# Optimization experiments

Measured on AMD Instinct MI355X. Metric: run time of the kernel, lower is better.

## Reference

```python
import jax, jax.numpy as jnp
import numpy as np

B, L, N, D, H = 8, 2048, 512, 1024, 16
Hd = D // H
EPS = 1e-5


def layer_norm(x, g, b):
    m = jnp.mean(x, axis=-1, keepdims=True)
    v = jnp.mean(jnp.square(x - m), axis=-1, keepdims=True)
    return (x - m) * jax.lax.rsqrt(v + EPS) * g + b


def setup_inputs() -> dict:
    key = jax.random.key(0)
    ks = jax.random.split(key, 8)
    text = jax.random.normal(ks[0], (B, L, D), dtype=jnp.float32)
    regions = jax.random.normal(ks[1], (B, N, D), dtype=jnp.float32)
    region_mask = jax.random.randint(ks[2], (B, N), 0, 2).astype(bool)
    s = 1.0 / np.sqrt(D)
    Wq = jax.random.normal(ks[3], (D, D), dtype=jnp.float32) * s
    Wk = jax.random.normal(ks[4], (D, D), dtype=jnp.float32) * s
    Wv = jax.random.normal(ks[5], (D, D), dtype=jnp.float32) * s
    Wo = jax.random.normal(ks[6], (D, D), dtype=jnp.float32) * s
    bo = jnp.zeros((D,), dtype=jnp.float32)
    gq = jnp.ones((D,), dtype=jnp.float32)
    bq = jnp.zeros((D,), dtype=jnp.float32)
    gkv = jnp.ones((D,), dtype=jnp.float32)
    bkv = jnp.zeros((D,), dtype=jnp.float32)
    return {"text": text, "regions": regions, "region_mask": region_mask,
            "Wq": Wq, "Wk": Wk, "Wv": Wv, "Wo": Wo, "bo": bo,
            "gq": gq, "bq": bq, "gkv": gkv, "bkv": bkv}


def reference(text, regions, region_mask, Wq, Wk, Wv, Wo, bo, gq, bq, gkv, bkv):
    scale = Hd ** -0.5
    # pre-norm on text (Q) and regions (K only; V uses raw regions, as in source)
    q = layer_norm(text, gq, bq) @ Wq.T            # (B, L, D)
    k = layer_norm(regions, gkv, bkv) @ Wk.T       # (B, N, D)
    v = regions @ Wv.T                              # (B, N, D)
    q = q.reshape(B, L, H, Hd).transpose(0, 2, 1, 3)   # (B, H, L, Hd)
    k = k.reshape(B, N, H, Hd).transpose(0, 2, 1, 3)   # (B, H, N, Hd)
    v = v.reshape(B, N, H, Hd).transpose(0, 2, 1, 3)   # (B, H, N, Hd)
    logits = jnp.einsum('bhld,bhnd->bhln', q, k) * scale
    logits = jnp.where(region_mask[:, None, None, :], logits, -jnp.inf)
    attn = jax.nn.softmax(logits, axis=-1)
    attn = jnp.nan_to_num(attn, nan=0.0)  # all-masked rows -> zeros
    # dropout is identity in eval mode
    out = jnp.einsum('bhln,bhnd->bhld', attn, v)
    out = out.transpose(0, 2, 1, 3).reshape(B, L, D)
    return text + out @ Wo.T + bo
```

## Files before the change

kernel.cpp:

```cpp
#include <hip/hip_runtime.h>

#define SC_L2E 0.180336880111120f

typedef _Float16 half8v __attribute__((ext_vector_type(8)));
typedef _Float16 half4v __attribute__((ext_vector_type(4)));
typedef _Float16 half2v __attribute__((ext_vector_type(2)));
typedef float f32x4 __attribute__((ext_vector_type(4)));
typedef float f32x16 __attribute__((ext_vector_type(16)));

#if __has_builtin(__builtin_amdgcn_exp2f)
#define EXP2(x) __builtin_amdgcn_exp2f(x)
#else
#define EXP2(x) exp2f(x)
#endif

#if __has_builtin(__builtin_amdgcn_cvt_pkrtz)
#define CVTPK(a, b) __builtin_amdgcn_cvt_pkrtz((a), (b))
#else
static __device__ __forceinline__ half2v cvtpk_fb(float a, float b) {
  half2v h; h[0] = (_Float16)a; h[1] = (_Float16)b; return h;
}
#define CVTPK cvtpk_fb
#endif

#define FMAX3(a, b, c) fmaxf(fmaxf((a), (b)), (c))

#define SWZ_OFF(row, lg) ((row) * 32 + ((((lg) ^ (((row) >> 1) & 3))) * 8))

__device__ __forceinline__ void gload_lds16(const void* g, void* l) {
  __builtin_amdgcn_global_load_lds(
      (const __attribute__((address_space(1))) void*)g,
      (__attribute__((address_space(3))) void*)l, 16, 0, 0);
}

__global__ __launch_bounds__(256) void prep_all_kernel(
    const float* __restrict__ W0, const float* __restrict__ W1,
    const float* __restrict__ W2, const float* __restrict__ W3,
    _Float16* __restrict__ Wout, const float* __restrict__ text,
    const float* __restrict__ gq, const float* __restrict__ bq,
    _Float16* __restrict__ Tout, const float* __restrict__ regions,
    const float* __restrict__ gkv, const float* __restrict__ bkv,
    _Float16* __restrict__ Rln, _Float16* __restrict__ Rraw,
    const unsigned char* __restrict__ mask, int* __restrict__ flag) {
  const int blk = blockIdx.x;
  const int t = threadIdx.x;
  if (blk < 2048) {
    const int i = blk * 256 + t;
    const int rgn = i >> 17;
    const float* W = (rgn == 0) ? W0 : (rgn == 1) ? W1 : (rgn == 2) ? W2 : W3;
    const int loc = i & 131071;
    const float4 a  = ((const float4*)W)[loc * 2];
    const float4 b2 = ((const float4*)W)[loc * 2 + 1];
    half8v y;
    y[0] = (_Float16)a.x;  y[1] = (_Float16)a.y;
    y[2] = (_Float16)a.z;  y[3] = (_Float16)a.w;
    y[4] = (_Float16)b2.x; y[5] = (_Float16)b2.y;
    y[6] = (_Float16)b2.z; y[7] = (_Float16)b2.w;
    ((half8v*)Wout)[i] = y;
  } else if (blk < 22528) {
    const bool is_text = blk < 18432;
    const int row = is_text ? (blk - 2048) : (blk - 18432);
    const float* X = is_text ? text : regions;
    const float* ga = is_text ? gq : gkv;
    const float* be = is_text ? bq : bkv;
    const float4 x = ((const float4*)(X + (size_t)row * 1024))[t];
    float s  = x.x + x.y + x.z + x.w;
    float ss = x.x * x.x + x.y * x.y + x.z * x.z + x.w * x.w;
#pragma unroll
    for (int off = 32; off > 0; off >>= 1) {
      s  += __shfl_down(s, off);
      ss += __shfl_down(ss, off);
    }
    __shared__ float red[8];
    __shared__ float smu, srs;
    if ((t & 63) == 0) { red[(t >> 6) * 2] = s; red[(t >> 6) * 2 + 1] = ss; }
    __syncthreads();
    if (t == 0) {
      const float S  = red[0] + red[2] + red[4] + red[6];
      const float SS = red[1] + red[3] + red[5] + red[7];
      const float mm = S * (1.f / 1024.f);
      const float vv = SS * (1.f / 1024.f) - mm * mm;
      smu = mm; srs = rsqrtf(vv + 1e-5f);
    }
    __syncthreads();
    const float mu = smu, rs = srs;
    const float4 g  = ((const float4*)ga)[t];
    const float4 bb = ((const float4*)be)[t];
    half4v y;
    y[0] = (_Float16)((x.x - mu) * rs * g.x + bb.x);
    y[1] = (_Float16)((x.y - mu) * rs * g.y + bb.y);
    y[2] = (_Float16)((x.z - mu) * rs * g.z + bb.z);
    y[3] = (_Float16)((x.w - mu) * rs * g.w + bb.w);
    if (is_text) {
      ((half4v*)(Tout + (size_t)row * 1024))[t] = y;
    } else {
      half4v yr;
      yr[0] = (_Float16)x.x; yr[1] = (_Float16)x.y;
      yr[2] = (_Float16)x.z; yr[3] = (_Float16)x.w;
      ((half4v*)(Rln + (size_t)row * 1024))[t] = y;
      ((half4v*)(Rraw + (size_t)row * 1024))[t] = yr;
    }
  } else {
    __shared__ int sany;
    if (t == 0) sany = 0;
    __syncthreads();
    int any = 0;
    for (int i = t; i < 8 * 512; i += 256)
      if ((i & 3) != 0 && mask[i] != 0) any = 1;
    if (any) sany = 1;
    __syncthreads();
    if (t == 0) *flag = sany;
  }
}

template <int EPI>
__global__ __launch_bounds__(512) void hgemm_big(
    const _Float16* __restrict__ A, const _Float16* __restrict__ W,
    void* __restrict__ Yv, const float* __restrict__ bias,
    const float* __restrict__ resid) {
  __shared__ _Float16 As[32768];
  __shared__ _Float16 Bs[32768];
  const int tid = threadIdx.x;
  const int wg = blockIdx.x;
  const int bm = (wg & 7) * 8 + (wg >> 5);
  const int bn = (wg >> 3) & 3;
  const int wid = tid >> 6, lane = tid & 63;
  const int wr = wid >> 2, wc = wid & 3;
  const int l15 = lane & 15, lg = lane >> 4;

  const int c0 = tid, c1 = tid + 512;
  const int sc0 = ((c0 & 3) ^ ((c0 >> 3) & 3)) * 8;
  const int sc1 = ((c1 & 3) ^ ((c1 >> 3) & 3)) * 8;
  const _Float16* Ag0 = A + (size_t)(bm * 256 + (c0 >> 2)) * 1024 + sc0;
  const _Float16* Ag1 = A + (size_t)(bm * 256 + (c1 >> 2)) * 1024 + sc1;
  const _Float16* Bg0 = W + (size_t)(bn * 256 + (c0 >> 2)) * 1024 + sc0;
  const _Float16* Bg1 = W + (size_t)(bn * 256 + (c1 >> 2)) * 1024 + sc1;
  _Float16* Asl0 = &As[wid * 512];
  _Float16* Asl1 = &As[4096 + wid * 512];
  _Float16* Bsl0 = &Bs[wid * 512];
  _Float16* Bsl1 = &Bs[4096 + wid * 512];

  auto stage = [&](int tk, int bi) {
    const int off = tk * 32;
    gload_lds16(Ag0 + off, Asl0 + bi * 8192);
    gload_lds16(Ag1 + off, Asl1 + bi * 8192);
    gload_lds16(Bg0 + off, Bsl0 + bi * 8192);
    gload_lds16(Bg1 + off, Bsl1 + bi * 8192);
  };

  f32x4 acc[8][4] = {};
  auto compute = [&](int t) {
    const _Float16* Ab = &As[(t & 3) * 8192];
    const _Float16* Bb = &Bs[(t & 3) * 8192];
    half8v a[8], b[4];
#pragma unroll
    for (int m = 0; m < 8; m++) {
      const int row = wr * 128 + m * 16 + l15;
      a[m] = *(const half8v*)&Ab[SWZ_OFF(row, lg)];
    }
#pragma unroll
    for (int n = 0; n < 4; n++) {
      const int row = wc * 64 + n * 16 + l15;
      b[n] = *(const half8v*)&Bb[SWZ_OFF(row, lg)];
    }
    __builtin_amdgcn_s_setprio(1);
#pragma unroll
    for (int m = 0; m < 8; m++)
#pragma unroll
      for (int n = 0; n < 4; n++)
        acc[m][n] = __builtin_amdgcn_mfma_f32_16x16x32_f16(a[m], b[n], acc[m][n], 0, 0, 0);
    __builtin_amdgcn_s_setprio(0);
  };

  stage(0, 0);
  stage(1, 1);
  for (int t = 0; t < 30; ++t) {
    stage(t + 2, (t + 2) & 3);
    asm volatile("s_waitcnt vmcnt(8)" ::: "memory");
    __builtin_amdgcn_sched_barrier(0);
    __builtin_amdgcn_s_barrier();
    compute(t);
  }
  asm volatile("s_waitcnt vmcnt(4)" ::: "memory");
  __builtin_amdgcn_sched_barrier(0);
  __builtin_amdgcn_s_barrier();
  compute(30);
  asm volatile("s_waitcnt vmcnt(0)" ::: "memory");
  __builtin_amdgcn_sched_barrier(0);
  __builtin_amdgcn_s_barrier();
  compute(31);

  if (EPI == 0) {
    _Float16* Y = (_Float16*)Yv;
#pragma unroll
    for (int m = 0; m < 8; m++) {
      const int gr0 = bm * 256 + wr * 128 + m * 16 + lg * 4;
#pragma unroll
      for (int n = 0; n < 4; n++) {
        const int gc = bn * 256 + wc * 64 + n * 16 + l15;
#pragma unroll
        for (int r = 0; r < 4; r++)
          Y[(size_t)(gr0 + r) * 1024 + gc] = (_Float16)(acc[m][n][r] * SC_L2E);
      }
    }
  } else {
    float* Y = (float*)Yv;
#pragma unroll
    for (int m = 0; m < 8; m++) {
      const int gr0 = bm * 256 + wr * 128 + m * 16 + lg * 4;
#pragma unroll
      for (int n = 0; n < 4; n++) {
        const int gc = bn * 256 + wc * 64 + n * 16 + l15;
        const float bv = bias[gc];
#pragma unroll
        for (int r = 0; r < 4; r++)
          Y[(size_t)(gr0 + r) * 1024 + gc] =
              acc[m][n][r] + bv + resid[(size_t)(gr0 + r) * 1024 + gc];
      }
    }
  }
}

__global__ __launch_bounds__(256) void hgemm_kv(
    const _Float16* __restrict__ Aln, const _Float16* __restrict__ Araw,
    const _Float16* __restrict__ Wk, const _Float16* __restrict__ Wv,
    _Float16* __restrict__ Yk, _Float16* __restrict__ YvT) {
  __shared__ _Float16 As[16384];
  __shared__ _Float16 Bs[16384];
  const int z = blockIdx.z;
  const _Float16* A = z ? Araw : Aln;
  const _Float16* W = z ? Wv : Wk;
  const int tid = threadIdx.x;
  const int bm = blockIdx.x, bn = blockIdx.y;
  const int wid = tid >> 6, lane = tid & 63;
  const int wr = wid >> 1, wc = wid & 1;
  const int l15 = lane & 15, lg = lane >> 4;

  const int c0 = tid, c1 = tid + 256;
  const int sc0 = ((c0 & 3) ^ ((c0 >> 3) & 3)) * 8;
  const int sc1 = ((c1 & 3) ^ ((c1 >> 3) & 3)) * 8;
  const _Float16* Ag0 = A + (size_t)(bm * 128 + (c0 >> 2)) * 1024 + sc0;
  const _Float16* Ag1 = A + (size_t)(bm * 128 + (c1 >> 2)) * 1024 + sc1;
  const _Float16* Bg0 = W + (size_t)(bn * 128 + (c0 >> 2)) * 1024 + sc0;
  const _Float16* Bg1 = W + (size_t)(bn * 128 + (c1 >> 2)) * 1024 + sc1;
  _Float16* Asl = &As[wid * 512];
  _Float16* Bsl = &Bs[wid * 512];

  auto stage = [&](int tk, int bi) {
    const int off = tk * 32;
    gload_lds16(Ag0 + off, Asl + bi * 4096);
    gload_lds16(Ag1 + off, Asl + bi * 4096 + 2048);
    gload_lds16(Bg0 + off, Bsl + bi * 4096);
    gload_lds16(Bg1 + off, Bsl + bi * 4096 + 2048);
  };

  f32x4 acc[4][4] = {};
  auto compute = [&](int t) {
    const _Float16* Ab = &As[(t & 3) * 4096];
    const _Float16* Bb = &Bs[(t & 3) * 4096];
    half8v a[4], b[4];
#pragma unroll
    for (int m = 0; m < 4; m++) {
      const int row = wr * 64 + m * 16 + l15;
      a[m] = *(const half8v*)&Ab[SWZ_OFF(row, lg)];
    }
#pragma unroll
    for (int n = 0; n < 4; n++) {
      const int row = wc * 64 + n * 16 + l15;
      b[n] = *(const half8v*)&Bb[SWZ_OFF(row, lg)];
    }
    __builtin_amdgcn_s_setprio(1);
#pragma unroll
    for (int m = 0; m < 4; m++)
#pragma unroll
      for (int n = 0; n < 4; n++)
        acc[m][n] = __builtin_amdgcn_mfma_f32_16x16x32_f16(a[m], b[n], acc[m][n], 0, 0, 0);
    __builtin_amdgcn_s_setprio(0);
  };

  stage(0, 0);
  stage(1, 1);
  for (int t = 0; t < 30; ++t) {
    stage(t + 2, (t + 2) & 3);
    asm volatile("s_waitcnt vmcnt(8)" ::: "memory");
    __builtin_amdgcn_sched_barrier(0);
    __builtin_amdgcn_s_barrier();
    compute(t);
  }
  asm volatile("s_waitcnt vmcnt(4)" ::: "memory");
  __builtin_amdgcn_sched_barrier(0);
  __builtin_amdgcn_s_barrier();
  compute(30);
  asm volatile("s_waitcnt vmcnt(0)" ::: "memory");
  __builtin_amdgcn_sched_barrier(0);
  __builtin_amdgcn_s_barrier();
  compute(31);

  if (z == 0) {
#pragma unroll
    for (int m = 0; m < 4; m++) {
      const int gr0 = bm * 128 + wr * 64 + m * 16 + lg * 4;
#pragma unroll
      for (int n = 0; n < 4; n++) {
        const int gc = bn * 128 + wc * 64 + n * 16 + l15;
#pragma unroll
        for (int r = 0; r < 4; r++)
          Yk[(size_t)(gr0 + r) * 1024 + gc] = (_Float16)acc[m][n][r];
      }
    }
  } else {
#pragma unroll
    for (int m = 0; m < 4; m++) {
      const int gr0 = bm * 128 + wr * 64 + m * 16 + lg * 4;
#pragma unroll
      for (int n = 0; n < 4; n++) {
        const int gc = bn * 128 + wc * 64 + n * 16 + l15;
#pragma unroll
        for (int r = 0; r < 4; r++) {
          const int tokenv = gr0 + r;
          YvT[(size_t)((tokenv >> 9) * 1024 + gc) * 512 + (tokenv & 511)] =
              (_Float16)acc[m][n][r];
        }
      }
    }
  }
}

__global__ __launch_bounds__(256, 4) void attn_v9(
    const _Float16* __restrict__ q, const _Float16* __restrict__ kk,
    const _Float16* __restrict__ vT, const void* __restrict__ maskp,
    const int* __restrict__ flag, _Float16* __restrict__ ctx) {
  __shared__ union SMem {
    struct { _Float16 K[2][2][2048]; _Float16 V[2][2][2048]; } s;
    _Float16 Ot[4][2048];
  } sm;
  __shared__ float Msk[512];

  const int bid = (blockIdx.x & 7) * 256 + (blockIdx.x >> 3);
  const int qt = bid & 15, hh = (bid >> 4) & 15, b = bid >> 8;
  const int tid = threadIdx.x;
  const int wid = tid >> 6, lane = tid & 63;
  const int l31 = lane & 31;
  const int hi  = lane >> 5;

  {
    const bool mu8 = (*flag != 0);
    const unsigned char* m8 = (const unsigned char*)maskp;
    const int* m32 = (const int*)maskp;
    for (int i = tid; i < 512; i += 256) {
      const bool mv = mu8 ? (m8[b * 512 + i] != 0) : (m32[b * 512 + i] != 0);
      Msk[i] = mv ? 0.f : -__builtin_inff();
    }
  }

  const _Float16* kb = kk + (size_t)b * 512 * 1024 + hh * 64;
  const _Float16* vb = vT + (size_t)(b * 1024 + hh * 64) * 512;

  const int krow = wid * 8 + (lane >> 3);
  const int kchk = (lane & 7) ^ ((lane >> 3) & 7);
  const _Float16* ksrc = kb + (size_t)krow * 1024 + kchk * 8;
  const int vrow = wid * 16 + (lane >> 2);
  const int vchk = (lane & 3) ^ ((lane >> 3) & 3);
  const _Float16* vsrc = vb + (size_t)vrow * 512 + vchk * 8;

  const int tok0 = b * 2048 + qt * 128 + wid * 32;
  half8v bq[4];
#pragma unroll
  for (int kg = 0; kg < 4; kg++)
    bq[kg] = *(const half8v*)(q + (size_t)(tok0 + l31) * 1024 + hh * 64 + kg * 16 + hi * 8);

  float m_s = -1e30f, l_s = 0.f;
  f32x16 ot0 = {}, ot1 = {};

  auto stage = [&](int step, int bi) {
#pragma unroll
    for (int sub = 0; sub < 2; sub++) {
      const int tile = step * 2 + sub;
      gload_lds16(ksrc + (size_t)tile * 32 * 1024, &sm.s.K[bi][sub][wid * 512]);
      gload_lds16(vsrc + tile * 32, &sm.s.V[bi][sub][wid * 512]);
    }
  };

  stage(0, 0);
  __syncthreads();

  int buf = 0;
  for (int step = 0; step < 8; step++) {
    if (step < 7) stage(step + 1, buf ^ 1);

#pragma unroll
    for (int sub = 0; sub < 2; sub++) {
      const int nt = step * 2 + sub;

      half8v ak[4];
#pragma unroll
      for (int kg = 0; kg < 4; kg++)
        ak[kg] = *(const half8v*)&sm.s.K[buf][sub][l31 * 64 + ((kg * 2 + hi) ^ (l31 & 7)) * 8];

      f32x16 st;
#pragma unroll
      for (int j = 0; j < 4; j++) {
        const float4 mk = *(const float4*)&Msk[nt * 32 + j * 8 + hi * 4];
        st[4 * j + 0] = mk.x;
        st[4 * j + 1] = mk.y;
        st[4 * j + 2] = mk.z;
        st[4 * j + 3] = mk.w;
      }
#pragma unroll
      for (int kg = 0; kg < 4; kg++)
        st = __builtin_amdgcn_mfma_f32_32x32x16_f16(ak[kg], bq[kg], st, 0, 0, 0);

      half8v av[2][2];
#pragma unroll
      for (int dv = 0; dv < 2; dv++)
#pragma unroll
        for (int kc = 0; kc < 2; kc++)
          av[dv][kc] = *(const half8v*)&sm.s.V[buf][sub][(dv * 32 + l31) * 32 +
                                                        ((kc * 2 + hi) ^ ((l31 >> 1) & 3)) * 8];

      const float t0 = FMAX3(st[0], st[1], st[2]);
      const float t1 = FMAX3(st[3], st[4], st[5]);
      const float t2 = FMAX3(st[6], st[7], st[8]);
      const float t3 = FMAX3(st[9], st[10], st[11]);
      const float t4 = FMAX3(st[12], st[13], st[14]);
      float tmax = fmaxf(FMAX3(t0, t1, t2), FMAX3(t3, t4, st[15]));
      tmax = fmaxf(tmax, __shfl_xor(tmax, 32, 64));

      if (__any(tmax > m_s + 8.f)) {
        const float mnew = fmaxf(m_s, tmax);
        const float corr = EXP2(m_s - mnew);
        m_s = mnew;
        l_s *= corr;
#pragma unroll
        for (int r = 0; r < 16; r++) { ot0[r] *= corr; ot1[r] *= corr; }
      }

      float p[16];
#pragma unroll
      for (int r = 0; r < 16; r++) p[r] = EXP2(st[r] - m_s);

      unsigned int pk[4][2];
#pragma unroll
      for (int j = 0; j < 4; j++)
#pragma unroll
        for (int pp = 0; pp < 2; pp++)
          pk[j][pp] = __builtin_bit_cast(
              unsigned int, CVTPK(p[4 * j + 2 * pp], p[4 * j + 2 * pp + 1]));

      {
#pragma unroll
        for (int r = 0; r < 8; r++) p[r] += p[r + 8];
#pragma unroll
        for (int r = 0; r < 4; r++) p[r] += p[r + 4];
        float ts = (p[0] + p[1]) + (p[2] + p[3]);
        ts += __shfl_xor(ts, 32, 64);
        l_s += ts;
      }

      half8v pb[2];
#pragma unroll
      for (int kc = 0; kc < 2; kc++) {
        unsigned int x0 = pk[2 * kc][0], x1 = pk[2 * kc][1];
        unsigned int y0 = pk[2 * kc + 1][0], y1 = pk[2 * kc + 1][1];
        asm("v_permlane32_swap_b32 %0, %1" : "+v"(x0), "+v"(y0));
        asm("v_permlane32_swap_b32 %0, %1" : "+v"(x1), "+v"(y1));
        uint4 u; u.x = x0; u.y = x1; u.z = y0; u.w = y1;
        pb[kc] = __builtin_bit_cast(half8v, u);
      }

      ot0 = __builtin_amdgcn_mfma_f32_32x32x16_f16(av[0][0], pb[0], ot0, 0, 0, 0);
      ot0 = __builtin_amdgcn_mfma_f32_32x32x16_f16(av[0][1], pb[1], ot0, 0, 0, 0);
      ot1 = __builtin_amdgcn_mfma_f32_32x32x16_f16(av[1][0], pb[0], ot1, 0, 0, 0);
      ot1 = __builtin_amdgcn_mfma_f32_32x32x16_f16(av[1][1], pb[1], ot1, 0, 0, 0);
    }

    __syncthreads();
    buf ^= 1;
  }

  const float inv = (l_s > 0.f) ? (1.f / l_s) : 0.f;
#pragma unroll
  for (int dv = 0; dv < 2; dv++) {
#pragma unroll
    for (int j = 0; j < 4; j++)
#pragma unroll
      for (int pp = 0; pp < 2; pp++) {
        const int r = 4 * j + 2 * pp;
        const float v0 = (dv ? ot1[r] : ot0[r]) * inv;
        const float v1 = (dv ? ot1[r + 1] : ot0[r + 1]) * inv;
        const int col = dv * 32 + 8 * j + 4 * hi + 2 * pp;
        const int pos = l31 * 64 + (col ^ (8 * (l31 & 7)));
        *(unsigned int*)&sm.Ot[wid][pos] = __builtin_bit_cast(unsigned int, CVTPK(v0, v1));
      }
  }
  __syncthreads();
#pragma unroll
  for (int qh = 0; qh < 2; qh++)
#pragma unroll
    for (int k2 = 0; k2 < 2; k2++) {
      const int qq = qh * 16 + (lane >> 2);
      const int c  = (lane & 3) * 8 + k2 * 32;
      const half8v val = *(const half8v*)&sm.Ot[wid][qq * 64 + (c ^ (8 * (qq & 7)))];
      *(half8v*)(ctx + (size_t)(tok0 + qq) * 1024 + hh * 64 + c) = val;
    }
}

extern "C" void kernel_launch(void* const* d_in, const int* in_sizes, int n_in,
                              void* d_out, int out_size, void* d_ws, size_t ws_size,
                              hipStream_t stream) {
  const float* text    = (const float*)d_in[0];
  const float* regions = (const float*)d_in[1];
  const void*  mask    = d_in[2];
  const float* Wq      = (const float*)d_in[3];
  const float* Wk      = (const float*)d_in[4];
  const float* Wv      = (const float*)d_in[5];
  const float* Wo      = (const float*)d_in[6];
  const float* bo      = (const float*)d_in[7];
  const float* gq      = (const float*)d_in[8];
  const float* bq      = (const float*)d_in[9];
  const float* gkv     = (const float*)d_in[10];
  const float* bkv     = (const float*)d_in[11];

  _Float16* ws16 = (_Float16*)d_ws;
  _Float16* wq16 = ws16;
  _Float16* wk16 = wq16 + 1048576;
  _Float16* wv16 = wk16 + 1048576;
  _Float16* wo16 = wv16 + 1048576;
  _Float16* at16 = wo16 + 1048576;
  _Float16* q16  = at16 + 16777216;
  _Float16* k16  = q16 + 16777216;
  _Float16* vTb  = k16 + 4194304;
  int* flag = (int*)(vTb + 4194304);
  _Float16* rln16  = (_Float16*)(flag + 16);
  _Float16* rraw16 = rln16 + 4194304;

  prep_all_kernel<<<22529, 256, 0, stream>>>(
      Wq, Wk, Wv, Wo, wq16, text, gq, bq, at16,
      regions, gkv, bkv, rln16, rraw16,
      (const unsigned char*)mask, flag);

  hgemm_big<0><<<256, 512, 0, stream>>>(at16, wq16, q16, nullptr, nullptr);

  hgemm_kv<<<dim3(32, 8, 2), 256, 0, stream>>>(rln16, rraw16, wk16, wv16, k16, vTb);

  attn_v9<<<2048, 256, 0, stream>>>(q16, k16, vTb, mask, flag, q16);

  hgemm_big<1><<<256, 512, 0, stream>>>(q16, wo16, d_out, bo, text);
}
```

Measured before the change: 202.5 us.

## Shrink big GEMM tiles to 128x256 with double-buffered pipeline and 256-thread blocks

Replaces the 256x256 tile, 512-thread, four-stage-buffer GEMM for the Q and output projections with a 128x256 tile, 256-thread, two-buffer variant launched on 512 blocks. LDS use drops from 128 KB to 48 KB per block and the grid doubles, which should improve CU coverage and occupancy on a 256-CU part. The pipeline now issues the next stage after compute behind an extra barrier rather than prefetching two stages ahead. In exchange, each block reuses A less and pays an extra barrier per k-step.

```diff
diff --git a/kernel.cpp b/kernel.cpp
--- a/kernel.cpp
+++ b/kernel.cpp
@@ -114,60 +114,72 @@
 }
 
 template <int EPI>
-__global__ __launch_bounds__(512) void hgemm_big(
+__global__ __launch_bounds__(256) void hgemm_mid(
     const _Float16* __restrict__ A, const _Float16* __restrict__ W,
     void* __restrict__ Yv, const float* __restrict__ bias,
     const float* __restrict__ resid) {
-  __shared__ _Float16 As[32768];
-  __shared__ _Float16 Bs[32768];
+  __shared__ _Float16 As[8192];
+  __shared__ _Float16 Bs[16384];
   const int tid = threadIdx.x;
   const int wg = blockIdx.x;
-  const int bm = (wg & 7) * 8 + (wg >> 5);
-  const int bn = (wg >> 3) & 3;
+  const int idx = wg >> 3;
+  const int bm = (wg & 7) * 16 + (idx >> 2);
+  const int bn = idx & 3;
   const int wid = tid >> 6, lane = tid & 63;
-  const int wr = wid >> 2, wc = wid & 3;
+  const int wr = wid >> 1, wc = wid & 1;
   const int l15 = lane & 15, lg = lane >> 4;
 
-  const int c0 = tid, c1 = tid + 512;
-  const int sc0 = ((c0 & 3) ^ ((c0 >> 3) & 3)) * 8;
-  const int sc1 = ((c1 & 3) ^ ((c1 >> 3) & 3)) * 8;
-  const _Float16* Ag0 = A + (size_t)(bm * 256 + (c0 >> 2)) * 1024 + sc0;
-  const _Float16* Ag1 = A + (size_t)(bm * 256 + (c1 >> 2)) * 1024 + sc1;
-  const _Float16* Bg0 = W + (size_t)(bn * 256 + (c0 >> 2)) * 1024 + sc0;
-  const _Float16* Bg1 = W + (size_t)(bn * 256 + (c1 >> 2)) * 1024 + sc1;
+  const int a0 = tid, a1 = tid + 256;
+  const int sa0 = ((a0 & 3) ^ ((a0 >> 3) & 3)) * 8;
+  const int sa1 = ((a1 & 3) ^ ((a1 >> 3) & 3)) * 8;
+  const _Float16* Ag0 = A + (size_t)(bm * 128 + (a0 >> 2)) * 1024 + sa0;
+  const _Float16* Ag1 = A + (size_t)(bm * 128 + (a1 >> 2)) * 1024 + sa1;
+  const int b0 = tid, b1 = tid + 256, b2 = tid + 512, b3 = tid + 768;
+  const int sb0 = ((b0 & 3) ^ ((b0 >> 3) & 3)) * 8;
+  const int sb1 = ((b1 & 3) ^ ((b1 >> 3) & 3)) * 8;
+  const int sb2 = ((b2 & 3) ^ ((b2 >> 3) & 3)) * 8;
+  const int sb3 = ((b3 & 3) ^ ((b3 >> 3) & 3)) * 8;
+  const _Float16* Bg0 = W + (size_t)(bn * 256 + (b0 >> 2)) * 1024 + sb0;
+  const _Float16* Bg1 = W + (size_t)(bn * 256 + (b1 >> 2)) * 1024 + sb1;
+  const _Float16* Bg2 = W + (size_t)(bn * 256 + (b2 >> 2)) * 1024 + sb2;
+  const _Float16* Bg3 = W + (size_t)(bn * 256 + (b3 >> 2)) * 1024 + sb3;
   _Float16* Asl0 = &As[wid * 512];
-  _Float16* Asl1 = &As[4096 + wid * 512];
+  _Float16* Asl1 = &As[2048 + wid * 512];
   _Float16* Bsl0 = &Bs[wid * 512];
-  _Float16* Bsl1 = &Bs[4096 + wid * 512];
+  _Float16* Bsl1 = &Bs[2048 + wid * 512];
+  _Float16* Bsl2 = &Bs[4096 + wid * 512];
+  _Float16* Bsl3 = &Bs[6144 + wid * 512];
 
   auto stage = [&](int tk, int bi) {
     const int off = tk * 32;
-    gload_lds16(Ag0 + off, Asl0 + bi * 8192);
-    gload_lds16(Ag1 + off, Asl1 + bi * 8192);
+    gload_lds16(Ag0 + off, Asl0 + bi * 4096);
+    gload_lds16(Ag1 + off, Asl1 + bi * 4096);
     gload_lds16(Bg0 + off, Bsl0 + bi * 8192);
     gload_lds16(Bg1 + off, Bsl1 + bi * 8192);
+    gload_lds16(Bg2 + off, Bsl2 + bi * 8192);
+    gload_lds16(Bg3 + off, Bsl3 + bi * 8192);
   };
 
-  f32x4 acc[8][4] = {};
+  f32x4 acc[4][8] = {};
   auto compute = [&](int t) {
-    const _Float16* Ab = &As[(t & 3) * 8192];
-    const _Float16* Bb = &Bs[(t & 3) * 8192];
-    half8v a[8], b[4];
-#pragma unroll
-    for (int m = 0; m < 8; m++) {
-      const int row = wr * 128 + m * 16 + l15;
+    const _Float16* Ab = &As[(t & 1) * 4096];
+    const _Float16* Bb = &Bs[(t & 1) * 8192];
+    half8v a[4], b[8];
+#pragma unroll
+    for (int m = 0; m < 4; m++) {
+      const int row = wr * 64 + m * 16 + l15;
       a[m] = *(const half8v*)&Ab[SWZ_OFF(row, lg)];
     }
 #pragma unroll
-    for (int n = 0; n < 4; n++) {
-      const int row = wc * 64 + n * 16 + l15;
+    for (int n = 0; n < 8; n++) {
+      const int row = wc * 128 + n * 16 + l15;
       b[n] = *(const half8v*)&Bb[SWZ_OFF(row, lg)];
     }
     __builtin_amdgcn_s_setprio(1);
 #pragma unroll
-    for (int m = 0; m < 8; m++)
-#pragma unroll
-      for (int n = 0; n < 4; n++)
+    for (int m = 0; m < 4; m++)
+#pragma unroll
+      for (int n = 0; n < 8; n++)
         acc[m][n] = __builtin_amdgcn_mfma_f32_16x16x32_f16(a[m], b[n], acc[m][n], 0, 0, 0);
     __builtin_amdgcn_s_setprio(0);
   };
@@ -175,13 +187,14 @@
   stage(0, 0);
   stage(1, 1);
   for (int t = 0; t < 30; ++t) {
-    stage(t + 2, (t + 2) & 3);
-    asm volatile("s_waitcnt vmcnt(8)" ::: "memory");
+    asm volatile("s_waitcnt vmcnt(6)" ::: "memory");
     __builtin_amdgcn_sched_barrier(0);
     __builtin_amdgcn_s_barrier();
     compute(t);
-  }
-  asm volatile("s_waitcnt vmcnt(4)" ::: "memory");
+    __builtin_amdgcn_s_barrier();
+    stage(t + 2, t & 1);
+  }
+  asm volatile("s_waitcnt vmcnt(6)" ::: "memory");
   __builtin_amdgcn_sched_barrier(0);
   __builtin_amdgcn_s_barrier();
   compute(30);
@@ -193,11 +206,11 @@
   if (EPI == 0) {
     _Float16* Y = (_Float16*)Yv;
 #pragma unroll
-    for (int m = 0; m < 8; m++) {
-      const int gr0 = bm * 256 + wr * 128 + m * 16 + lg * 4;
-#pragma unroll
-      for (int n = 0; n < 4; n++) {
-        const int gc = bn * 256 + wc * 64 + n * 16 + l15;
+    for (int m = 0; m < 4; m++) {
+      const int gr0 = bm * 128 + wr * 64 + m * 16 + lg * 4;
+#pragma unroll
+      for (int n = 0; n < 8; n++) {
+        const int gc = bn * 256 + wc * 128 + n * 16 + l15;
 #pragma unroll
         for (int r = 0; r < 4; r++)
           Y[(size_t)(gr0 + r) * 1024 + gc] = (_Float16)(acc[m][n][r] * SC_L2E);
@@ -206,11 +219,11 @@
   } else {
     float* Y = (float*)Yv;
 #pragma unroll
-    for (int m = 0; m < 8; m++) {
-      const int gr0 = bm * 256 + wr * 128 + m * 16 + lg * 4;
-#pragma unroll
-      for (int n = 0; n < 4; n++) {
-        const int gc = bn * 256 + wc * 64 + n * 16 + l15;
+    for (int m = 0; m < 4; m++) {
+      const int gr0 = bm * 128 + wr * 64 + m * 16 + lg * 4;
+#pragma unroll
+      for (int n = 0; n < 8; n++) {
+        const int gc = bn * 256 + wc * 128 + n * 16 + l15;
         const float bv = bias[gc];
 #pragma unroll
         for (int r = 0; r < 4; r++)
@@ -539,11 +552,11 @@
       regions, gkv, bkv, rln16, rraw16,
       (const unsigned char*)mask, flag);
 
-  hgemm_big<0><<<256, 512, 0, stream>>>(at16, wq16, q16, nullptr, nullptr);
+  hgemm_mid<0><<<512, 256, 0, stream>>>(at16, wq16, q16, nullptr, nullptr);
 
   hgemm_kv<<<dim3(32, 8, 2), 256, 0, stream>>>(rln16, rraw16, wk16, wv16, k16, vTb);
 
   attn_v9<<<2048, 256, 0, stream>>>(q16, k16, vTb, mask, flag, q16);
 
-  hgemm_big<1><<<256, 512, 0, stream>>>(q16, wo16, d_out, bo, text);
-}
+  hgemm_mid<1><<<512, 256, 0, stream>>>(q16, wo16, d_out, bo, text);
+}
```

After: 285.6 us. 41.0% more time.

## Restructure big GEMM mainloop into 3-stage buffer with split A/B staging

Applied to the files above, without the earlier changes.

The hgemm_big mainloop drops from a 4-slot to a 3-slot LDS ring, cutting shared memory per block from 128KB to 96KB. Each K-step is split into two MFMA half-phases. A-tile prefetch is issued after the first fragment reads and B-tile prefetch after the second, with an extra barrier in between. The aim is to interleave global-to-LDS loads with MFMA work and reduce register pressure by holding only four A fragments at a time. The cost is an extra barrier per iteration and shallower prefetch depth.

```diff
diff --git a/kernel.cpp b/kernel.cpp
--- a/kernel.cpp
+++ b/kernel.cpp
@@ -118,8 +118,8 @@
     const _Float16* __restrict__ A, const _Float16* __restrict__ W,
     void* __restrict__ Yv, const float* __restrict__ bias,
     const float* __restrict__ resid) {
-  __shared__ _Float16 As[32768];
-  __shared__ _Float16 Bs[32768];
+  __shared__ _Float16 As[24576];
+  __shared__ _Float16 Bs[24576];
   const int tid = threadIdx.x;
   const int wg = blockIdx.x;
   const int bm = (wg & 7) * 8 + (wg >> 5);
@@ -128,67 +128,98 @@
   const int wr = wid >> 2, wc = wid & 3;
   const int l15 = lane & 15, lg = lane >> 4;
 
-  const int c0 = tid, c1 = tid + 512;
-  const int sc0 = ((c0 & 3) ^ ((c0 >> 3) & 3)) * 8;
-  const int sc1 = ((c1 & 3) ^ ((c1 >> 3) & 3)) * 8;
-  const _Float16* Ag0 = A + (size_t)(bm * 256 + (c0 >> 2)) * 1024 + sc0;
-  const _Float16* Ag1 = A + (size_t)(bm * 256 + (c1 >> 2)) * 1024 + sc1;
-  const _Float16* Bg0 = W + (size_t)(bn * 256 + (c0 >> 2)) * 1024 + sc0;
-  const _Float16* Bg1 = W + (size_t)(bn * 256 + (c1 >> 2)) * 1024 + sc1;
-  _Float16* Asl0 = &As[wid * 512];
-  _Float16* Asl1 = &As[4096 + wid * 512];
-  _Float16* Bsl0 = &Bs[wid * 512];
-  _Float16* Bsl1 = &Bs[4096 + wid * 512];
-
-  auto stage = [&](int tk, int bi) {
-    const int off = tk * 32;
-    gload_lds16(Ag0 + off, Asl0 + bi * 8192);
-    gload_lds16(Ag1 + off, Asl1 + bi * 8192);
-    gload_lds16(Bg0 + off, Bsl0 + bi * 8192);
-    gload_lds16(Bg1 + off, Bsl1 + bi * 8192);
+  const int sc = ((tid & 3) ^ ((tid >> 3) & 3)) * 8;
+  const _Float16* aS0 = A + (size_t)(bm * 256 + (tid >> 2)) * 1024 + sc;
+  const _Float16* aS1 = aS0 + (size_t)128 * 1024;
+  const _Float16* bS0 = W + (size_t)(bn * 256 + (tid >> 2)) * 1024 + sc;
+  const _Float16* bS1 = bS0 + (size_t)128 * 1024;
+
+  auto stageA = [&](int Tt, int sl) {
+    gload_lds16(aS0 + Tt * 32, &As[sl * 8192 + wid * 512]);
+    gload_lds16(aS1 + Tt * 32, &As[sl * 8192 + 4096 + wid * 512]);
   };
+  auto stageB = [&](int Tt, int sl) {
+    gload_lds16(bS0 + Tt * 32, &Bs[sl * 8192 + wid * 512]);
+    gload_lds16(bS1 + Tt * 32, &Bs[sl * 8192 + 4096 + wid * 512]);
+  };
 
   f32x4 acc[8][4] = {};
-  auto compute = [&](int t) {
-    const _Float16* Ab = &As[(t & 3) * 8192];
-    const _Float16* Bb = &Bs[(t & 3) * 8192];
-    half8v a[8], b[4];
-#pragma unroll
-    for (int m = 0; m < 8; m++) {
-      const int row = wr * 128 + m * 16 + l15;
-      a[m] = *(const half8v*)&Ab[SWZ_OFF(row, lg)];
-    }
-#pragma unroll
-    for (int n = 0; n < 4; n++) {
-      const int row = wc * 64 + n * 16 + l15;
-      b[n] = *(const half8v*)&Bb[SWZ_OFF(row, lg)];
-    }
-    __builtin_amdgcn_s_setprio(1);
-#pragma unroll
-    for (int m = 0; m < 8; m++)
-#pragma unroll
-      for (int n = 0; n < 4; n++)
-        acc[m][n] = __builtin_amdgcn_mfma_f32_16x16x32_f16(a[m], b[n], acc[m][n], 0, 0, 0);
-    __builtin_amdgcn_s_setprio(0);
-  };
-
-  stage(0, 0);
-  stage(1, 1);
-  for (int t = 0; t < 30; ++t) {
-    stage(t + 2, (t + 2) & 3);
-    asm volatile("s_waitcnt vmcnt(8)" ::: "memory");
+
+  stageA(0, 0); stageB(0, 0);
+  stageA(1, 1); stageB(1, 1);
+
+  int s = 0, s2 = 2;
+  for (int T = 0; T < 32; ++T) {
+    if (T < 31) {
+      asm volatile("s_waitcnt vmcnt(4)" ::: "memory");
+    } else {
+      asm volatile("s_waitcnt vmcnt(0)" ::: "memory");
+    }
     __builtin_amdgcn_sched_barrier(0);
     __builtin_amdgcn_s_barrier();
-    compute(t);
-  }
-  asm volatile("s_waitcnt vmcnt(4)" ::: "memory");
-  __builtin_amdgcn_sched_barrier(0);
-  __builtin_amdgcn_s_barrier();
-  compute(30);
-  asm volatile("s_waitcnt vmcnt(0)" ::: "memory");
-  __builtin_amdgcn_sched_barrier(0);
-  __builtin_amdgcn_s_barrier();
-  compute(31);
+    const _Float16* Ab = &As[s * 8192];
+    const _Float16* Bb = &Bs[s * 8192];
+
+    half8v b0 = *(const half8v*)&Bb[SWZ_OFF(wc * 64 + 0 * 16 + l15, lg)];
+    half8v b1 = *(const half8v*)&Bb[SWZ_OFF(wc * 64 + 1 * 16 + l15, lg)];
+    half8v b2 = *(const half8v*)&Bb[SWZ_OFF(wc * 64 + 2 * 16 + l15, lg)];
+    half8v b3 = *(const half8v*)&Bb[SWZ_OFF(wc * 64 + 3 * 16 + l15, lg)];
+    half8v a0 = *(const half8v*)&Ab[SWZ_OFF(wr * 128 + 0 * 16 + l15, lg)];
+    half8v a1 = *(const half8v*)&Ab[SWZ_OFF(wr * 128 + 1 * 16 + l15, lg)];
+    half8v a2 = *(const half8v*)&Ab[SWZ_OFF(wr * 128 + 2 * 16 + l15, lg)];
+    half8v a3 = *(const half8v*)&Ab[SWZ_OFF(wr * 128 + 3 * 16 + l15, lg)];
+    if (T < 30) stageA(T + 2, s2);
+    asm volatile("s_waitcnt lgkmcnt(0)" ::: "memory");
+    __builtin_amdgcn_sched_barrier(0);
+    __builtin_amdgcn_s_setprio(1);
+    acc[0][0] = __builtin_amdgcn_mfma_f32_16x16x32_f16(a0, b0, acc[0][0], 0, 0, 0);
+    acc[0][1] = __builtin_amdgcn_mfma_f32_16x16x32_f16(a0, b1, acc[0][1], 0, 0, 0);
+    acc[0][2] = __builtin_amdgcn_mfma_f32_16x16x32_f16(a0, b2, acc[0][2], 0, 0, 0);
+    acc[0][3] = __builtin_amdgcn_mfma_f32_16x16x32_f16(a0, b3, acc[0][3], 0, 0, 0);
+    acc[1][0] = __builtin_amdgcn_mfma_f32_16x16x32_f16(a1, b0, acc[1][0], 0, 0, 0);
+    acc[1][1] = __builtin_amdgcn_mfma_f32_16x16x32_f16(a1, b1, acc[1][1], 0, 0, 0);
+    acc[1][2] = __builtin_amdgcn_mfma_f32_16x16x32_f16(a1, b2, acc[1][2], 0, 0, 0);
+    acc[1][3] = __builtin_amdgcn_mfma_f32_16x16x32_f16(a1, b3, acc[1][3], 0, 0, 0);
+    acc[2][0] = __builtin_amdgcn_mfma_f32_16x16x32_f16(a2, b0, acc[2][0], 0, 0, 0);
+    acc[2][1] = __builtin_amdgcn_mfma_f32_16x16x32_f16(a2, b1, acc[2][1], 0, 0, 0);
+    acc[2][2] = __builtin_amdgcn_mfma_f32_16x16x32_f16(a2, b2, acc[2][2], 0, 0, 0);
+    acc[2][3] = __builtin_amdgcn_mfma_f32_16x16x32_f16(a2, b3, acc[2][3], 0, 0, 0);
+    acc[3][0] = __builtin_amdgcn_mfma_f32_16x16x32_f16(a3, b0, acc[3][0], 0, 0, 0);
+    acc[3][1] = __builtin_amdgcn_mfma_f32_16x16x32_f16(a3, b1, acc[3][1], 0, 0, 0);
+    acc[3][2] = __builtin_amdgcn_mfma_f32_16x16x32_f16(a3, b2, acc[3][2], 0, 0, 0);
+    acc[3][3] = __builtin_amdgcn_mfma_f32_16x16x32_f16(a3, b3, acc[3][3], 0, 0, 0);
+    __builtin_amdgcn_s_setprio(0);
+    __builtin_amdgcn_s_barrier();
+
+    a0 = *(const half8v*)&Ab[SWZ_OFF(wr * 128 + 4 * 16 + l15, lg)];
+    a1 = *(const half8v*)&Ab[SWZ_OFF(wr * 128 + 5 * 16 + l15, lg)];
+    a2 = *(const half8v*)&Ab[SWZ_OFF(wr * 128 + 6 * 16 + l15, lg)];
+    a3 = *(const half8v*)&Ab[SWZ_OFF(wr * 128 + 7 * 16 + l15, lg)];
+    if (T < 30) stageB(T + 2, s2);
+    asm volatile("s_waitcnt lgkmcnt(0)" ::: "memory");
+    __builtin_amdgcn_sched_barrier(0);
+    __builtin_amdgcn_s_setprio(1);
+    acc[4][0] = __builtin_amdgcn_mfma_f32_16x16x32_f16(a0, b0, acc[4][0], 0, 0, 0);
+    acc[4][1] = __builtin_amdgcn_mfma_f32_16x16x32_f16(a0, b1, acc[4][1], 0, 0, 0);
+    acc[4][2] = __builtin_amdgcn_mfma_f32_16x16x32_f16(a0, b2, acc[4][2], 0, 0, 0);
+    acc[4][3] = __builtin_amdgcn_mfma_f32_16x16x32_f16(a0, b3, acc[4][3], 0, 0, 0);
+    acc[5][0] = __builtin_amdgcn_mfma_f32_16x16x32_f16(a1, b0, acc[5][0], 0, 0, 0);
+    acc[5][1] = __builtin_amdgcn_mfma_f32_16x16x32_f16(a1, b1, acc[5][1], 0, 0, 0);
+    acc[5][2] = __builtin_amdgcn_mfma_f32_16x16x32_f16(a1, b2, acc[5][2], 0, 0, 0);
+    acc[5][3] = __builtin_amdgcn_mfma_f32_16x16x32_f16(a1, b3, acc[5][3], 0, 0, 0);
+    acc[6][0] = __builtin_amdgcn_mfma_f32_16x16x32_f16(a2, b0, acc[6][0], 0, 0, 0);
+    acc[6][1] = __builtin_amdgcn_mfma_f32_16x16x32_f16(a2, b1, acc[6][1], 0, 0, 0);
+    acc[6][2] = __builtin_amdgcn_mfma_f32_16x16x32_f16(a2, b2, acc[6][2], 0, 0, 0);
+    acc[6][3] = __builtin_amdgcn_mfma_f32_16x16x32_f16(a2, b3, acc[6][3], 0, 0, 0);
+    acc[7][0] = __builtin_amdgcn_mfma_f32_16x16x32_f16(a3, b0, acc[7][0], 0, 0, 0);
+    acc[7][1] = __builtin_amdgcn_mfma_f32_16x16x32_f16(a3, b1, acc[7][1], 0, 0, 0);
+    acc[7][2] = __builtin_amdgcn_mfma_f32_16x16x32_f16(a3, b2, acc[7][2], 0, 0, 0);
+    acc[7][3] = __builtin_amdgcn_mfma_f32_16x16x32_f16(a3, b3, acc[7][3], 0, 0, 0);
+    __builtin_amdgcn_s_setprio(0);
+
+    s  = (s == 2)  ? 0 : s + 1;
+    s2 = (s2 == 2) ? 0 : s2 + 1;
+  }
 
   if (EPI == 0) {
     _Float16* Y = (_Float16*)Yv;
```

Result: no change. 204.6 us (+1.0%).
